# Performance work log

Measured on AMD Instinct MI355X. Metric: run time of the kernel, lower is better.

The kernel has to match this reference:

```python
import jax, jax.numpy as jnp
import numpy as np

EPS = 1e-07
NUM_CLASSES = 46


def setup_inputs() -> dict:
    key = jax.random.key(0)
    k1, k2 = jax.random.split(key)
    N = 2_000_000
    y_pred = jax.random.uniform(k1, (N, NUM_CLASSES), dtype=jnp.float32)
    y_true = jax.random.randint(k2, (N,), 0, NUM_CLASSES, dtype=jnp.int64)
    return {"y_pred": y_pred, "y_true": y_true}


def reference(y_pred, y_true):
    # One fused pass replacing the 46-iteration Python loop.
    # onehot[n, c] = 1 if y_true[n] == c
    classes = jnp.arange(NUM_CLASSES, dtype=y_true.dtype)
    onehot = (y_true[:, None] == classes[None, :]).astype(y_pred.dtype)  # [N, C]

    col_sum = jnp.sum(y_pred, axis=0)                 # [C] = tp + fp per class
    tp = jnp.sum(onehot * y_pred, axis=0)             # [C]
    counts = jnp.sum(onehot, axis=0)                  # [C] = tp + fn per class

    fp = col_sum - tp
    fn = counts - tp

    precision = tp / (tp + fp + EPS)
    recall = tp / (tp + fn + EPS)
    f1 = 2.0 * precision * recall / (precision + recall + EPS)
    f1 = jnp.clip(f1, EPS, 1.0 - EPS)
    return 1.0 - jnp.mean(f1)
```

## Files before the change

### kernel.cpp

```cpp
#include <hip/hip_runtime.h>

#define EPSF 1e-7f
#define NCLS 46
#define BLOCK 256
#define GRID (23 * 72)

__global__ __launch_bounds__(BLOCK) void f1_partial(
    const float* __restrict__ yp,
    const int* __restrict__ yt,
    float* __restrict__ g_cs,
    float* __restrict__ g_tp,
    float* __restrict__ g_cnt,
    int n_rows)
{
    __shared__ float s_cs[NCLS], s_tp[NCLS], s_cnt[NCLS];
    const int tid = threadIdx.x;
    for (int i = tid; i < NCLS; i += BLOCK) { s_cs[i] = 0.f; s_tp[i] = 0.f; s_cnt[i] = 0.f; }
    __syncthreads();

    const int T  = BLOCK * GRID;
    const int t  = blockIdx.x * BLOCK + tid;
    const int s        = t % 23;
    const int rp0      = t / 23;
    const int rpstride = T / 23;
    const int npairs   = n_rows >> 1;

    int cls[4], hi[4];
    #pragma unroll
    for (int j = 0; j < 4; ++j) {
        int e  = 4 * s + j;
        hi[j]  = (e >= 46) ? 1 : 0;
        cls[j] = e - 46 * hi[j];
    }

    float cs[4] = {0.f,0.f,0.f,0.f};
    float tp[4] = {0.f,0.f,0.f,0.f};

    for (int rp = rp0; rp < npairs; rp += rpstride) {
        float4 v = *(const float4*)(yp + rp * 92 + 4 * s);
        int2 lab = *(const int2*)(yt + 2 * rp);
        float vv[4] = {v.x, v.y, v.z, v.w};
        #pragma unroll
        for (int j = 0; j < 4; ++j) {
            cs[j] += vv[j];
            int labj = hi[j] ? lab.y : lab.x;
            tp[j] += (labj == cls[j]) ? vv[j] : 0.f;
        }
    }

    #pragma unroll
    for (int j = 0; j < 4; ++j) {
        atomicAdd(&s_cs[cls[j]], cs[j]);
        atomicAdd(&s_tp[cls[j]], tp[j]);
    }

    for (int i = t; i < n_rows; i += T)
        atomicAdd(&s_cnt[yt[i]], 1.0f);

    if ((n_rows & 1) && blockIdx.x == 0 && tid < NCLS) {
        int L = n_rows - 1;
        float v = yp[L * NCLS + tid];
        atomicAdd(&s_cs[tid], v);
        if (yt[L] == tid) atomicAdd(&s_tp[tid], v);
    }

    __syncthreads();
    for (int i = tid; i < NCLS; i += BLOCK) {
        atomicAdd(&g_cs[i],  s_cs[i]);
        atomicAdd(&g_tp[i],  s_tp[i]);
        atomicAdd(&g_cnt[i], s_cnt[i]);
    }
}

__global__ void f1_final(const float* __restrict__ g_cs,
                         const float* __restrict__ g_tp,
                         const float* __restrict__ g_cnt,
                         float* __restrict__ out)
{
    const int lane = threadIdx.x;
    float f1 = 0.f;
    if (lane < NCLS) {
        float tp = g_tp[lane];
        float p  = tp / (g_cs[lane]  + EPSF);
        float r  = tp / (g_cnt[lane] + EPSF);
        float f  = 2.0f * p * r / (p + r + EPSF);
        f1 = fminf(fmaxf(f, EPSF), 1.0f - EPSF);
    }
    #pragma unroll
    for (int off = 32; off > 0; off >>= 1)
        f1 += __shfl_down(f1, off);
    if (lane == 0)
        out[0] = 1.0f - f1 * (1.0f / 46.0f);
}

extern "C" void kernel_launch(void* const* d_in, const int* in_sizes, int n_in,
                              void* d_out, int out_size, void* d_ws, size_t ws_size,
                              hipStream_t stream)
{
    const float* yp = (const float*)d_in[0];
    const int* yt   = (const int*)d_in[1];
    const int n_rows = in_sizes[1];

    float* g_cs  = (float*)d_ws;
    float* g_tp  = g_cs + NCLS;
    float* g_cnt = g_tp + NCLS;

    hipMemsetAsync(d_ws, 0, 3 * NCLS * sizeof(float), stream);
    f1_partial<<<GRID, BLOCK, 0, stream>>>(yp, yt, g_cs, g_tp, g_cnt, n_rows);
    f1_final<<<1, 64, 0, stream>>>(g_cs, g_tp, g_cnt, (float*)d_out);
}
```

Baseline: 524.1 us.

## Fuse finalize into partial kernel via last-block counter and fold label counting

Merges the finalize kernel into the reduction kernel using a global completion counter, so the last block to finish computes the F1 loss, removing one kernel launch. Label counts are now accumulated inside the main loop by the s==0 lane from the labels it already loaded, dropping the separate pass that re-read y_true. The main loads of y_pred become nontemporal and the grid grows from 23*72 to 23*88 blocks. In exchange it adds a threadfence and a global atomic per block, plus shared atomics from one lane per row pair during the hot loop.

```diff
diff --git a/kernel.cpp b/kernel.cpp
--- a/kernel.cpp
+++ b/kernel.cpp
@@ -3,17 +3,22 @@
 #define EPSF 1e-7f
 #define NCLS 46
 #define BLOCK 256
-#define GRID (23 * 72)
+#define GRID (23 * 88)
 
-__global__ __launch_bounds__(BLOCK) void f1_partial(
+typedef float f32x4 __attribute__((ext_vector_type(4)));
+
+__global__ __launch_bounds__(BLOCK) void f1_fused(
     const float* __restrict__ yp,
-    const int* __restrict__ yt,
-    float* __restrict__ g_cs,
-    float* __restrict__ g_tp,
-    float* __restrict__ g_cnt,
+    const int*   __restrict__ yt,
+    float*       __restrict__ g_cs,
+    float*       __restrict__ g_tp,
+    float*       __restrict__ g_cnt,
+    unsigned*    __restrict__ g_done,
+    float*       __restrict__ out,
     int n_rows)
 {
     __shared__ float s_cs[NCLS], s_tp[NCLS], s_cnt[NCLS];
+    __shared__ int s_last;
     const int tid = threadIdx.x;
     for (int i = tid; i < NCLS; i += BLOCK) { s_cs[i] = 0.f; s_tp[i] = 0.f; s_cnt[i] = 0.f; }
     __syncthreads();
@@ -29,15 +34,16 @@
     #pragma unroll
     for (int j = 0; j < 4; ++j) {
         int e  = 4 * s + j;
-        hi[j]  = (e >= 46) ? 1 : 0;
-        cls[j] = e - 46 * hi[j];
+        hi[j]  = (e >= NCLS) ? 1 : 0;
+        cls[j] = e - NCLS * hi[j];
     }
 
-    float cs[4] = {0.f,0.f,0.f,0.f};
-    float tp[4] = {0.f,0.f,0.f,0.f};
+    float cs[4] = {0.f, 0.f, 0.f, 0.f};
+    float tp[4] = {0.f, 0.f, 0.f, 0.f};
 
     for (int rp = rp0; rp < npairs; rp += rpstride) {
-        float4 v = *(const float4*)(yp + rp * 92 + 4 * s);
+        f32x4 v = __builtin_nontemporal_load(
+                      (const f32x4*)(yp + (size_t)rp * 92 + 4 * s));
         int2 lab = *(const int2*)(yt + 2 * rp);
         float vv[4] = {v.x, v.y, v.z, v.w};
         #pragma unroll
@@ -45,6 +51,10 @@
             cs[j] += vv[j];
             int labj = hi[j] ? lab.y : lab.x;
             tp[j] += (labj == cls[j]) ? vv[j] : 0.f;
+        }
+        if (s == 0) {
+            atomicAdd(&s_cnt[lab.x], 1.f);
+            atomicAdd(&s_cnt[lab.y], 1.f);
         }
     }
 
@@ -54,14 +64,15 @@
         atomicAdd(&s_tp[cls[j]], tp[j]);
     }
 
-    for (int i = t; i < n_rows; i += T)
-        atomicAdd(&s_cnt[yt[i]], 1.0f);
-
-    if ((n_rows & 1) && blockIdx.x == 0 && tid < NCLS) {
+    if ((n_rows & 1) && blockIdx.x == 0 && tid <= NCLS) {
         int L = n_rows - 1;
-        float v = yp[L * NCLS + tid];
-        atomicAdd(&s_cs[tid], v);
-        if (yt[L] == tid) atomicAdd(&s_tp[tid], v);
+        if (tid < NCLS) {
+            float v = yp[(size_t)L * NCLS + tid];
+            atomicAdd(&s_cs[tid], v);
+            if (yt[L] == tid) atomicAdd(&s_tp[tid], v);
+        } else {
+            atomicAdd(&s_cnt[yt[L]], 1.f);
+        }
     }
 
     __syncthreads();
@@ -70,27 +81,30 @@
         atomicAdd(&g_tp[i],  s_tp[i]);
         atomicAdd(&g_cnt[i], s_cnt[i]);
     }
-}
 
-__global__ void f1_final(const float* __restrict__ g_cs,
-                         const float* __restrict__ g_tp,
-                         const float* __restrict__ g_cnt,
-                         float* __restrict__ out)
-{
-    const int lane = threadIdx.x;
-    float f1 = 0.f;
-    if (lane < NCLS) {
-        float tp = g_tp[lane];
-        float p  = tp / (g_cs[lane]  + EPSF);
-        float r  = tp / (g_cnt[lane] + EPSF);
-        float f  = 2.0f * p * r / (p + r + EPSF);
-        f1 = fminf(fmaxf(f, EPSF), 1.0f - EPSF);
+    __threadfence();
+    if (tid == 0) {
+        unsigned prev = atomicAdd(g_done, 1u);
+        s_last = (prev == (unsigned)(GRID - 1));
     }
-    #pragma unroll
-    for (int off = 32; off > 0; off >>= 1)
-        f1 += __shfl_down(f1, off);
-    if (lane == 0)
-        out[0] = 1.0f - f1 * (1.0f / 46.0f);
+    __syncthreads();
+    if (s_last && tid < 64) {
+        float f1 = 0.f;
+        if (tid < NCLS) {
+            float tpv = atomicAdd(&g_tp[tid],  0.f);
+            float csv = atomicAdd(&g_cs[tid],  0.f);
+            float cnv = atomicAdd(&g_cnt[tid], 0.f);
+            float p = tpv / (csv + EPSF);
+            float r = tpv / (cnv + EPSF);
+            float f = 2.0f * p * r / (p + r + EPSF);
+            f1 = fminf(fmaxf(f, EPSF), 1.0f - EPSF);
+        }
+        #pragma unroll
+        for (int off = 32; off > 0; off >>= 1)
+            f1 += __shfl_down(f1, off);
+        if (tid == 0)
+            out[0] = 1.0f - f1 * (1.0f / 46.0f);
+    }
 }
 
 extern "C" void kernel_launch(void* const* d_in, const int* in_sizes, int n_in,
@@ -101,11 +115,12 @@
     const int* yt   = (const int*)d_in[1];
     const int n_rows = in_sizes[1];
 
-    float* g_cs  = (float*)d_ws;
-    float* g_tp  = g_cs + NCLS;
-    float* g_cnt = g_tp + NCLS;
+    float* g_cs      = (float*)d_ws;
+    float* g_tp      = g_cs + NCLS;
+    float* g_cnt     = g_tp + NCLS;
+    unsigned* g_done = (unsigned*)(g_cnt + NCLS);
 
-    hipMemsetAsync(d_ws, 0, 3 * NCLS * sizeof(float), stream);
-    f1_partial<<<GRID, BLOCK, 0, stream>>>(yp, yt, g_cs, g_tp, g_cnt, n_rows);
-    f1_final<<<1, 64, 0, stream>>>(g_cs, g_tp, g_cnt, (float*)d_out);
+    hipMemsetAsync(d_ws, 0, (3 * NCLS + 1) * sizeof(float), stream);
+    f1_fused<<<GRID, BLOCK, 0, stream>>>(yp, yt, g_cs, g_tp, g_cnt, g_done,
+                                         (float*)d_out, n_rows);
 }
```

After: 632.3 us. 20.6% more time.
